# Kernel tuning notes

Measured on AMD Instinct MI355X. Metric: run time of the kernel, lower is better.

## Reference

```python
import jax, jax.numpy as jnp
import numpy as np

N, E = 50000, 600000
NODE_DIM, EDGE_DIM, MSG_DIM = 128, 64, 128


def setup_inputs() -> dict:
    key = jax.random.key(0)
    ks = jax.random.split(key, 8)
    s = 0.05
    return {
        "node_features": jax.random.normal(ks[0], (N, NODE_DIM), jnp.float32),
        "edge_features": jax.random.normal(ks[1], (E, EDGE_DIM), jnp.float32),
        "edge_index": jax.random.randint(ks[2], (2, E), 0, N, jnp.int32),
        "We1": jax.random.normal(ks[3], (2 * NODE_DIM + EDGE_DIM, 32), jnp.float32) * s,
        "be1": jnp.zeros((32,), jnp.float32),
        "We2": jax.random.normal(ks[4], (32, MSG_DIM), jnp.float32) * s,
        "be2": jnp.zeros((MSG_DIM,), jnp.float32),
        "Wn1": jax.random.normal(ks[5], (NODE_DIM + MSG_DIM, 64), jnp.float32) * s,
        "bn1": jnp.zeros((64,), jnp.float32),
        "Wn2": jax.random.normal(ks[6], (64, MSG_DIM), jnp.float32) * s,
        "bn2": jnp.zeros((MSG_DIM,), jnp.float32),
    }


def reference(node_features, edge_features, edge_index,
              We1, be1, We2, be2, Wn1, bn1, Wn2, bn2):
    src, dst = edge_index[0], edge_index[1]
    src_f = node_features[src]            # [E, node_dim] gather
    dst_f = node_features[dst]            # [E, node_dim] gather
    # edge message encoder: 2-layer MLP with ReLU
    edge_in = jnp.concatenate([src_f, dst_f, edge_features], axis=1)  # [E, 2*nd+ed]
    h = jax.nn.relu(edge_in @ We1 + be1)
    edge_msg = jax.nn.relu(h @ We2 + be2)  # [E, msg_dim]
    # node message encoder
    node_in = jnp.concatenate([dst_f, edge_msg], axis=1)  # [E, nd+md]
    h2 = jax.nn.relu(node_in @ Wn1 + bn1)
    node_msg = jax.nn.relu(h2 @ Wn2 + bn2)  # [E, msg_dim]
    # scatter-sum over destination nodes (replaces the O(N) python loop)
    agg = jax.ops.segment_sum(node_msg, dst, num_segments=node_features.shape[0])
    return node_features + agg
```

## Files before the change

### kernel.cpp

```cpp
#include <hip/hip_runtime.h>
#include <hip/hip_bf16.h>

constexpr int N_NODES = 50000;
constexpr int N_EDGES = 600000;
constexpr int ND = 128;
constexpr int ED = 64;
constexpr int MD = 128;
constexpr int H1 = 32;
constexpr int H2 = 64;

typedef __attribute__((ext_vector_type(8))) short short8;
typedef __attribute__((ext_vector_type(4))) float f32x4;

#define MFMA16(a, b, c) __builtin_amdgcn_mfma_f32_16x16x32_bf16((a), (b), (c), 0, 0, 0)

constexpr size_t WS_MSGS    = 0;
constexpr size_t WS_PRE     = WS_MSGS + (size_t)N_EDGES * MD * 2;
constexpr size_t WS_POS     = WS_PRE + (size_t)N_NODES * 128 * 2;
constexpr size_t WS_COUNTS  = WS_POS + (size_t)N_EDGES * 4;
constexpr size_t WS_OFFSETS = WS_COUNTS + (size_t)N_NODES * 4;
constexpr size_t WS_WFE     = ((WS_OFFSETS + (size_t)(N_NODES + 1) * 4 + 15) / 16) * 16;
constexpr size_t WS_WFN     = WS_WFE + (size_t)44 * 64 * 16;
constexpr size_t WS_END     = WS_WFN + (size_t)32 * 64 * 16;

__device__ inline float bflo(unsigned u) { return __uint_as_float(u << 16); }
__device__ inline float bfhi(unsigned u) { return __uint_as_float(u & 0xffff0000u); }
__device__ inline float bf2f(unsigned short v) { return __uint_as_float((unsigned)v << 16); }
__device__ inline short f2bf(float f) {
    __hip_bfloat16 h = __float2bfloat16(f);
    return *reinterpret_cast<short*>(&h);
}

__global__ __launch_bounds__(256) void wprep(
    const float* __restrict__ We1, const float* __restrict__ We2,
    const float* __restrict__ Wn1, const float* __restrict__ Wn2,
    short8* __restrict__ wfE, short8* __restrict__ wfN)
{
    const int g = blockIdx.x * 256 + threadIdx.x;
    const int lane = g & 63;
    const int f = g >> 6;
    const int m16 = lane & 15, quad = lane >> 4;
    short v[8];
    if (f < 44) {
        #pragma unroll
        for (int j = 0; j < 8; ++j) {
            const int kq = quad * 8 + j;
            float s;
            if (f < 4) {
                const int kt = f >> 1, nt = f & 1;
                s = We1[(size_t)(2 * ND + kt * 32 + kq) * H1 + nt * 16 + m16];
            } else if (f < 12) {
                const int nt = f - 4;
                s = We2[(size_t)kq * MD + nt * 16 + m16];
            } else if (f < 28) {
                const int ff = f - 12, kt = ff >> 2, nt = ff & 3;
                s = Wn1[(size_t)(ND + kt * 32 + kq) * H2 + nt * 16 + m16];
            } else {
                const int ff = f - 28, kt = ff >> 3, nt = ff & 7;
                s = Wn2[(size_t)(kt * 32 + kq) * MD + nt * 16 + m16];
            }
            v[j] = f2bf(s);
        }
        wfE[g] = short8{v[0], v[1], v[2], v[3], v[4], v[5], v[6], v[7]};
    } else {
        const int ff = f - 44, kt = ff >> 3, nt = ff & 7;
        const int n = nt * 16 + m16;
        #pragma unroll
        for (int j = 0; j < 8; ++j) {
            const int k = kt * 32 + quad * 8 + j;
            float s;
            if (n < 32)      s = We1[(size_t)k * H1 + n];
            else if (n < 64) s = We1[(size_t)(ND + k) * H1 + (n - 32)];
            else             s = Wn1[(size_t)k * H2 + (n - 64)];
            v[j] = f2bf(s);
        }
        wfN[(size_t)(f - 44) * 64 + lane] = short8{v[0], v[1], v[2], v[3], v[4], v[5], v[6], v[7]};
    }
}

__global__ __launch_bounds__(256) void hist_pos(const int* __restrict__ eidx,
                                                int* __restrict__ counts,
                                                int* __restrict__ pos) {
    const int e = blockIdx.x * 256 + threadIdx.x;
    if (e < N_EDGES) pos[e] = atomicAdd(&counts[eidx[N_EDGES + e]], 1);
}

__global__ __launch_bounds__(1024) void scan_kernel(const int* __restrict__ counts,
                                                    int* __restrict__ offsets) {
    constexpr int T = 1024;
    constexpr int CHUNK = (N_NODES + T - 1) / T;
    const int tid = threadIdx.x;
    const int base = tid * CHUNK;
    int s = 0;
    #pragma unroll
    for (int i = 0; i < CHUNK; ++i) {
        const int idx = base + i;
        if (idx < N_NODES) s += counts[idx];
    }
    __shared__ int sm[T];
    sm[tid] = s;
    __syncthreads();
    for (int off = 1; off < T; off <<= 1) {
        const int v = (tid >= off) ? sm[tid - off] : 0;
        __syncthreads();
        sm[tid] += v;
        __syncthreads();
    }
    int run = sm[tid] - s;
    #pragma unroll
    for (int i = 0; i < CHUNK; ++i) {
        const int idx = base + i;
        if (idx < N_NODES) {
            offsets[idx] = run;
            run += counts[idx];
        }
    }
    if (tid == T - 1) offsets[N_NODES] = sm[T - 1];
}

__global__ __launch_bounds__(256) void node_pre_mfma(
    const float* __restrict__ nf, const short8* __restrict__ wfN,
    unsigned short* __restrict__ pre)
{
    __shared__ short ost[4][2048];
    const int tid = threadIdx.x;
    const int w = tid >> 6, lane = tid & 63;
    const int m16 = lane & 15, quad = lane >> 4;
    const int n0 = blockIdx.x * 64 + w * 16;

    short8 a[4];
    #pragma unroll
    for (int kt = 0; kt < 4; ++kt) {
        const int node = min(n0 + m16, N_NODES - 1);
        const float* pn = nf + (size_t)node * ND + kt * 32 + quad * 8;
        const float4 f0 = *(const float4*)pn;
        const float4 f1 = *(const float4*)(pn + 4);
        a[kt] = short8{f2bf(f0.x), f2bf(f0.y), f2bf(f0.z), f2bf(f0.w),
                       f2bf(f1.x), f2bf(f1.y), f2bf(f1.z), f2bf(f1.w)};
    }
    f32x4 acc[8];
    #pragma unroll
    for (int nt = 0; nt < 8; ++nt) acc[nt] = f32x4{0.f, 0.f, 0.f, 0.f};
    #pragma unroll
    for (int kt = 0; kt < 4; ++kt) {
        #pragma unroll
        for (int nt = 0; nt < 8; ++nt)
            acc[nt] = MFMA16(a[kt], wfN[(size_t)(kt * 8 + nt) * 64 + lane], acc[nt]);
    }
    short* o = &ost[w][0];
    #pragma unroll
    for (int nt = 0; nt < 8; ++nt)
        #pragma unroll
        for (int r = 0; r < 4; ++r)
            o[(quad * 4 + r) * 128 + nt * 16 + m16] = f2bf(acc[nt][r]);
    asm volatile("s_waitcnt lgkmcnt(0)" ::: "memory");
    #pragma unroll
    for (int i = 0; i < 4; ++i) {
        const int row = i * 4 + quad;
        const int node = n0 + row;
        if (node < N_NODES) {
            const uint4 v = ((const uint4*)(o + row * 128))[m16];
            *((uint4*)(pre + (size_t)node * 128) + m16) = v;
        }
    }
}

__global__ __launch_bounds__(256, 4) void edge_mfma(
    const float* __restrict__ ef, const int* __restrict__ eidx,
    const unsigned short* __restrict__ pre,
    const int* __restrict__ pos, const int* __restrict__ offsets,
    const short8* __restrict__ wfE,
    const float* __restrict__ be1, const float* __restrict__ be2,
    const float* __restrict__ bn1, const float* __restrict__ bn2,
    unsigned short* __restrict__ msgs)
{
    constexpr int TE = 64;
    __shared__ float l1init[TE][36];
    __shared__ unsigned short a3lds[TE][72];
    __shared__ int slotlds[TE];
    __shared__ short wbufB[4][2176];

    const int tid = threadIdx.x;
    const int e0 = blockIdx.x * TE;
    const int w = tid >> 6, lane = tid & 63;
    const int m16 = lane & 15, quad = lane >> 4;
    const int er0 = w * 16;

    float4 efv0, efv1, efv2, efv3;
    {
        const float* pe = ef + (size_t)(e0 + er0 + m16) * ED + quad * 8;
        efv0 = *(const float4*)pe;
        efv1 = *(const float4*)(pe + 4);
        efv2 = *(const float4*)(pe + 32);
        efv3 = *(const float4*)(pe + 36);
    }
    float bias2[8], bias3[4], bias4[8];
    #pragma unroll
    for (int nt = 0; nt < 8; ++nt) bias2[nt] = be2[nt * 16 + m16];
    #pragma unroll
    for (int nt = 0; nt < 4; ++nt) bias3[nt] = bn1[nt * 16 + m16];
    #pragma unroll
    for (int nt = 0; nt < 8; ++nt) bias4[nt] = bn2[nt * 16 + m16];

    {
        const int et = tid >> 2, p = tid & 3;
        const int e = e0 + et;
        const int src = eidx[e];
        const int dst = eidx[N_EDGES + e];
        const uint4* pa = (const uint4*)(pre + (size_t)src * 128);
        const uint4* pd = (const uint4*)(pre + (size_t)dst * 128);
        const uint4 ua = pa[p];
        const uint4 ud = pd[4 + p];
        const uint4 s0 = pd[8 + 2 * p];
        const uint4 s1 = pd[9 + 2 * p];
        const float4 b0 = ((const float4*)be1)[2 * p];
        const float4 b1 = ((const float4*)be1)[2 * p + 1];
        float4 r0, r1;
        r0.x = bflo(ua.x) + bflo(ud.x) + b0.x;
        r0.y = bfhi(ua.x) + bfhi(ud.x) + b0.y;
        r0.z = bflo(ua.y) + bflo(ud.y) + b0.z;
        r0.w = bfhi(ua.y) + bfhi(ud.y) + b0.w;
        r1.x = bflo(ua.z) + bflo(ud.z) + b1.x;
        r1.y = bfhi(ua.z) + bfhi(ud.z) + b1.y;
        r1.z = bflo(ua.w) + bflo(ud.w) + b1.z;
        r1.w = bfhi(ua.w) + bfhi(ud.w) + b1.w;
        float4* o = (float4*)&l1init[et][p * 8];
        o[0] = r0; o[1] = r1;
        uint4* oa = (uint4*)&a3lds[et][p * 16];
        oa[0] = s0; oa[1] = s1;
        const int sl = offsets[dst] + pos[e];
        if (p == 3) slotlds[et] = sl;
    }
    asm volatile("s_waitcnt lgkmcnt(0)" ::: "memory");

    short8 aef0 = short8{f2bf(efv0.x), f2bf(efv0.y), f2bf(efv0.z), f2bf(efv0.w),
                         f2bf(efv1.x), f2bf(efv1.y), f2bf(efv1.z), f2bf(efv1.w)};
    short8 aef1 = short8{f2bf(efv2.x), f2bf(efv2.y), f2bf(efv2.z), f2bf(efv2.w),
                         f2bf(efv3.x), f2bf(efv3.y), f2bf(efv3.z), f2bf(efv3.w)};

    short* alb = (short*)&l1init[er0][0];
    short* msb = &wbufB[w][0];

    f32x4 acc1[2];
    #pragma unroll
    for (int nt = 0; nt < 2; ++nt)
        #pragma unroll
        for (int r = 0; r < 4; ++r)
            acc1[nt][r] = l1init[er0 + quad * 4 + r][nt * 16 + m16];
    #pragma unroll
    for (int nt = 0; nt < 2; ++nt) {
        acc1[nt] = MFMA16(aef0, wfE[(size_t)(0 * 2 + nt) * 64 + lane], acc1[nt]);
        acc1[nt] = MFMA16(aef1, wfE[(size_t)(1 * 2 + nt) * 64 + lane], acc1[nt]);
    }
    #pragma unroll
    for (int nt = 0; nt < 2; ++nt)
        #pragma unroll
        for (int r = 0; r < 4; ++r)
            alb[(quad * 4 + r) * 40 + nt * 16 + m16] = f2bf(fmaxf(acc1[nt][r], 0.0f));
    asm volatile("s_waitcnt lgkmcnt(0)" ::: "memory");

    const short8 ah = *(const short8*)(alb + m16 * 40 + quad * 8);
    f32x4 acc2[8];
    #pragma unroll
    for (int nt = 0; nt < 8; ++nt) {
        acc2[nt] = f32x4{bias2[nt], bias2[nt], bias2[nt], bias2[nt]};
        acc2[nt] = MFMA16(ah, wfE[(size_t)(4 + nt) * 64 + lane], acc2[nt]);
    }
    #pragma unroll
    for (int nt = 0; nt < 8; ++nt)
        #pragma unroll
        for (int r = 0; r < 4; ++r)
            msb[(quad * 4 + r) * 136 + nt * 16 + m16] = f2bf(fmaxf(acc2[nt][r], 0.0f));
    asm volatile("s_waitcnt lgkmcnt(0)" ::: "memory");

    short8 am[4];
    #pragma unroll
    for (int kt = 0; kt < 4; ++kt)
        am[kt] = *(const short8*)(msb + m16 * 136 + kt * 32 + quad * 8);
    f32x4 acc3[4];
    #pragma unroll
    for (int nt = 0; nt < 4; ++nt)
        #pragma unroll
        for (int r = 0; r < 4; ++r)
            acc3[nt][r] = bias3[nt] + bf2f(a3lds[er0 + quad * 4 + r][nt * 16 + m16]);
    #pragma unroll
    for (int kt = 0; kt < 4; ++kt) {
        #pragma unroll
        for (int nt = 0; nt < 4; ++nt)
            acc3[nt] = MFMA16(am[kt], wfE[(size_t)(12 + kt * 4 + nt) * 64 + lane], acc3[nt]);
    }
    #pragma unroll
    for (int nt = 0; nt < 4; ++nt)
        #pragma unroll
        for (int r = 0; r < 4; ++r)
            alb[(quad * 4 + r) * 72 + nt * 16 + m16] = f2bf(fmaxf(acc3[nt][r], 0.0f));
    asm volatile("s_waitcnt lgkmcnt(0)" ::: "memory");

    short8 a4[2];
    #pragma unroll
    for (int kt = 0; kt < 2; ++kt)
        a4[kt] = *(const short8*)(alb + m16 * 72 + kt * 32 + quad * 8);
    f32x4 acc4[8];
    #pragma unroll
    for (int nt = 0; nt < 8; ++nt)
        acc4[nt] = f32x4{bias4[nt], bias4[nt], bias4[nt], bias4[nt]};
    #pragma unroll
    for (int kt = 0; kt < 2; ++kt) {
        #pragma unroll
        for (int nt = 0; nt < 8; ++nt)
            acc4[nt] = MFMA16(a4[kt], wfE[(size_t)(28 + kt * 8 + nt) * 64 + lane], acc4[nt]);
    }
    #pragma unroll
    for (int nt = 0; nt < 8; ++nt)
        #pragma unroll
        for (int r = 0; r < 4; ++r)
            msb[(quad * 4 + r) * 128 + nt * 16 + m16] = f2bf(fmaxf(acc4[nt][r], 0.0f));
    asm volatile("s_waitcnt lgkmcnt(0)" ::: "memory");

    #pragma unroll
    for (int i = 0; i < 4; ++i) {
        const int row = i * 4 + quad;
        const int sl = slotlds[er0 + row];
        const uint4 v = ((const uint4*)(msb + row * 128))[m16];
        *((uint4*)(msgs + (size_t)sl * 128) + m16) = v;
    }
}

__global__ __launch_bounds__(256) void gather2(
    const float* __restrict__ nf,
    const uint4* __restrict__ msgs4,
    const int* __restrict__ offsets,
    float* __restrict__ out)
{
    const int node = blockIdx.x * 16 + (threadIdx.x >> 4);
    const int m16 = threadIdx.x & 15;

    const float4* pn = (const float4*)(nf + (size_t)node * ND) + m16 * 2;
    const float4 n0 = pn[0];
    const float4 n1 = pn[1];

    const int beg = offsets[node];
    const int end = offsets[node + 1];

    float4 s0 = float4{0.f, 0.f, 0.f, 0.f};
    float4 s1 = float4{0.f, 0.f, 0.f, 0.f};
    const uint4* p = msgs4 + (size_t)beg * 16 + m16;
    int i = beg;
    for (; i + 1 < end; i += 2, p += 32) {
        const uint4 u0 = p[0];
        const uint4 u1 = p[16];
        s0.x += bflo(u0.x); s0.y += bfhi(u0.x);
        s0.z += bflo(u0.y); s0.w += bfhi(u0.y);
        s1.x += bflo(u0.z); s1.y += bfhi(u0.z);
        s1.z += bflo(u0.w); s1.w += bfhi(u0.w);
        s0.x += bflo(u1.x); s0.y += bfhi(u1.x);
        s0.z += bflo(u1.y); s0.w += bfhi(u1.y);
        s1.x += bflo(u1.z); s1.y += bfhi(u1.z);
        s1.z += bflo(u1.w); s1.w += bfhi(u1.w);
    }
    if (i < end) {
        const uint4 u = p[0];
        s0.x += bflo(u.x); s0.y += bfhi(u.x);
        s0.z += bflo(u.y); s0.w += bfhi(u.y);
        s1.x += bflo(u.z); s1.y += bfhi(u.z);
        s1.z += bflo(u.w); s1.w += bfhi(u.w);
    }
    s0.x += n0.x; s0.y += n0.y; s0.z += n0.z; s0.w += n0.w;
    s1.x += n1.x; s1.y += n1.y; s1.z += n1.z; s1.w += n1.w;

    float4* po = (float4*)(out + (size_t)node * ND) + m16 * 2;
    po[0] = s0;
    po[1] = s1;
}

extern "C" void kernel_launch(void* const* d_in, const int* in_sizes, int n_in,
                              void* d_out, int out_size, void* d_ws, size_t ws_size,
                              hipStream_t stream) {
    const float* nf  = (const float*)d_in[0];
    const float* ef  = (const float*)d_in[1];
    const int*  eidx = (const int*)d_in[2];
    const float* We1 = (const float*)d_in[3];
    const float* be1 = (const float*)d_in[4];
    const float* We2 = (const float*)d_in[5];
    const float* be2 = (const float*)d_in[6];
    const float* Wn1 = (const float*)d_in[7];
    const float* bn1 = (const float*)d_in[8];
    const float* Wn2 = (const float*)d_in[9];
    const float* bn2 = (const float*)d_in[10];
    float* out = (float*)d_out;

    char* ws = (char*)d_ws;
    unsigned short* msgs = (unsigned short*)(ws + WS_MSGS);
    unsigned short* pre  = (unsigned short*)(ws + WS_PRE);
    int* pos             = (int*)(ws + WS_POS);
    int* counts          = (int*)(ws + WS_COUNTS);
    int* offsets         = (int*)(ws + WS_OFFSETS);
    short8* wfE          = (short8*)(ws + WS_WFE);
    short8* wfN          = (short8*)(ws + WS_WFN);
    (void)ws_size; (void)WS_END;

    hipMemsetAsync(counts, 0, (size_t)N_NODES * 4, stream);
    wprep<<<19, 256, 0, stream>>>(We1, We2, Wn1, Wn2, wfE, wfN);
    hist_pos<<<(N_EDGES + 255) / 256, 256, 0, stream>>>(eidx, counts, pos);
    scan_kernel<<<1, 1024, 0, stream>>>(counts, offsets);
    node_pre_mfma<<<(N_NODES + 63) / 64, 256, 0, stream>>>(nf, wfN, pre);
    edge_mfma<<<N_EDGES / 64, 256, 0, stream>>>(
        ef, eidx, pre, pos, offsets, wfE, be1, be2, bn1, bn2, msgs);
    gather2<<<N_NODES / 16, 256, 0, stream>>>(nf, (const uint4*)msgs, offsets, out);
}
```

Measured before the change: 494.4 us.

## Transpose edge MLP MFMAs to keep activations in registers between layers

The edge MLP now swaps the MFMA operand roles: weights become the A operand and activations the B operand. Combined with a permuted K ordering of the weights in wprep, each layer's ReLU'd output feeds the next layer directly from registers instead of round-tripping through LDS. This cuts LDS traffic, waitcnts and shared memory, and occupancy is raised to 5 waves per SIMD. Packed bf16 conversion instructions replace scalar conversions. The scan is vectorised with padded counts, at the cost of tighter register pressure and a more intricate index mapping.

```diff
diff --git a/kernel.cpp b/kernel.cpp
--- a/kernel.cpp
+++ b/kernel.cpp
@@ -11,24 +11,41 @@
 
 typedef __attribute__((ext_vector_type(8))) short short8;
 typedef __attribute__((ext_vector_type(4))) float f32x4;
+typedef __attribute__((ext_vector_type(4))) unsigned int uint32x4;
 
 #define MFMA16(a, b, c) __builtin_amdgcn_mfma_f32_16x16x32_bf16((a), (b), (c), 0, 0, 0)
 
+constexpr int COUNTS_PAD = 53248;
 constexpr size_t WS_MSGS    = 0;
 constexpr size_t WS_PRE     = WS_MSGS + (size_t)N_EDGES * MD * 2;
 constexpr size_t WS_POS     = WS_PRE + (size_t)N_NODES * 128 * 2;
 constexpr size_t WS_COUNTS  = WS_POS + (size_t)N_EDGES * 4;
-constexpr size_t WS_OFFSETS = WS_COUNTS + (size_t)N_NODES * 4;
+constexpr size_t WS_OFFSETS = WS_COUNTS + (size_t)COUNTS_PAD * 4;
 constexpr size_t WS_WFE     = ((WS_OFFSETS + (size_t)(N_NODES + 1) * 4 + 15) / 16) * 16;
 constexpr size_t WS_WFN     = WS_WFE + (size_t)44 * 64 * 16;
 constexpr size_t WS_END     = WS_WFN + (size_t)32 * 64 * 16;
 
 __device__ inline float bflo(unsigned u) { return __uint_as_float(u << 16); }
 __device__ inline float bfhi(unsigned u) { return __uint_as_float(u & 0xffff0000u); }
-__device__ inline float bf2f(unsigned short v) { return __uint_as_float((unsigned)v << 16); }
 __device__ inline short f2bf(float f) {
     __hip_bfloat16 h = __float2bfloat16(f);
     return *reinterpret_cast<short*>(&h);
+}
+__device__ inline unsigned pkbf(float a, float b) {
+    unsigned r;
+    asm("v_cvt_pk_bf16_f32 %0, %1, %2" : "=v"(r) : "v"(a), "v"(b));
+    return r;
+}
+__device__ inline unsigned prelu(float a, float b) {
+    return pkbf(fmaxf(a, 0.0f), fmaxf(b, 0.0f));
+}
+__device__ inline short8 pack8(unsigned w0, unsigned w1, unsigned w2, unsigned w3) {
+    uint32x4 t{w0, w1, w2, w3};
+    return __builtin_bit_cast(short8, t);
+}
+
+__device__ inline int hperm(int kt, int kq) {
+    return (kt * 2 + ((kq >> 2) & 1)) * 16 + ((kq >> 3) & 3) * 4 + (kq & 3);
 }
 
 __global__ __launch_bounds__(256) void wprep(
@@ -47,17 +64,17 @@
             const int kq = quad * 8 + j;
             float s;
             if (f < 4) {
-                const int kt = f >> 1, nt = f & 1;
-                s = We1[(size_t)(2 * ND + kt * 32 + kq) * H1 + nt * 16 + m16];
+                const int kt = f >> 1, mt = f & 1;
+                s = We1[(size_t)(2 * ND + kt * 32 + kq) * H1 + mt * 16 + m16];
             } else if (f < 12) {
-                const int nt = f - 4;
-                s = We2[(size_t)kq * MD + nt * 16 + m16];
+                const int mt = f - 4;
+                s = We2[(size_t)hperm(0, kq) * MD + mt * 16 + m16];
             } else if (f < 28) {
-                const int ff = f - 12, kt = ff >> 2, nt = ff & 3;
-                s = Wn1[(size_t)(ND + kt * 32 + kq) * H2 + nt * 16 + m16];
+                const int ff = f - 12, kt = ff >> 2, mt = ff & 3;
+                s = Wn1[(size_t)(ND + hperm(kt, kq)) * H2 + mt * 16 + m16];
             } else {
-                const int ff = f - 28, kt = ff >> 3, nt = ff & 7;
-                s = Wn2[(size_t)(kt * 32 + kq) * MD + nt * 16 + m16];
+                const int ff = f - 28, kt = ff >> 3, mt = ff & 7;
+                s = Wn2[(size_t)hperm(kt, kq) * MD + mt * 16 + m16];
             }
             v[j] = f2bf(s);
         }
@@ -88,34 +105,35 @@
 __global__ __launch_bounds__(1024) void scan_kernel(const int* __restrict__ counts,
                                                     int* __restrict__ offsets) {
     constexpr int T = 1024;
-    constexpr int CHUNK = (N_NODES + T - 1) / T;
+    constexpr int CHUNK = 52;
     const int tid = threadIdx.x;
     const int base = tid * CHUNK;
+    int4 v[13];
     int s = 0;
-    #pragma unroll
-    for (int i = 0; i < CHUNK; ++i) {
-        const int idx = base + i;
-        if (idx < N_NODES) s += counts[idx];
+    const int4* pc = (const int4*)(counts + base);
+    #pragma unroll
+    for (int i = 0; i < 13; ++i) {
+        v[i] = pc[i];
+        s += v[i].x + v[i].y + v[i].z + v[i].w;
     }
     __shared__ int sm[T];
     sm[tid] = s;
     __syncthreads();
     for (int off = 1; off < T; off <<= 1) {
-        const int v = (tid >= off) ? sm[tid - off] : 0;
+        const int t = (tid >= off) ? sm[tid - off] : 0;
         __syncthreads();
-        sm[tid] += v;
+        sm[tid] += t;
         __syncthreads();
     }
     int run = sm[tid] - s;
     #pragma unroll
-    for (int i = 0; i < CHUNK; ++i) {
-        const int idx = base + i;
-        if (idx < N_NODES) {
-            offsets[idx] = run;
-            run += counts[idx];
-        }
-    }
-    if (tid == T - 1) offsets[N_NODES] = sm[T - 1];
+    for (int i = 0; i < 13; ++i) {
+        const int idx = base + i * 4;
+        if (idx     <= N_NODES) offsets[idx]     = run;  run += v[i].x;
+        if (idx + 1 <= N_NODES) offsets[idx + 1] = run;  run += v[i].y;
+        if (idx + 2 <= N_NODES) offsets[idx + 2] = run;  run += v[i].z;
+        if (idx + 3 <= N_NODES) offsets[idx + 3] = run;  run += v[i].w;
+    }
 }
 
 __global__ __launch_bounds__(256) void node_pre_mfma(
@@ -135,8 +153,8 @@
         const float* pn = nf + (size_t)node * ND + kt * 32 + quad * 8;
         const float4 f0 = *(const float4*)pn;
         const float4 f1 = *(const float4*)(pn + 4);
-        a[kt] = short8{f2bf(f0.x), f2bf(f0.y), f2bf(f0.z), f2bf(f0.w),
-                       f2bf(f1.x), f2bf(f1.y), f2bf(f1.z), f2bf(f1.w)};
+        a[kt] = pack8(pkbf(f0.x, f0.y), pkbf(f0.z, f0.w),
+                      pkbf(f1.x, f1.y), pkbf(f1.z, f1.w));
     }
     f32x4 acc[8];
     #pragma unroll
@@ -165,7 +183,7 @@
     }
 }
 
-__global__ __launch_bounds__(256, 4) void edge_mfma(
+__global__ __launch_bounds__(256, 5) void edge_mfma(
     const float* __restrict__ ef, const int* __restrict__ eidx,
     const unsigned short* __restrict__ pre,
     const int* __restrict__ pos, const int* __restrict__ offsets,
@@ -175,32 +193,24 @@
     unsigned short* __restrict__ msgs)
 {
     constexpr int TE = 64;
-    __shared__ float l1init[TE][36];
-    __shared__ unsigned short a3lds[TE][72];
+    __shared__ __align__(16) char sws[4][4608];
     __shared__ int slotlds[TE];
-    __shared__ short wbufB[4][2176];
 
     const int tid = threadIdx.x;
     const int e0 = blockIdx.x * TE;
     const int w = tid >> 6, lane = tid & 63;
-    const int m16 = lane & 15, quad = lane >> 4;
+    const int m16 = lane & 15, q = lane >> 4;
     const int er0 = w * 16;
+    char* swsb = &sws[w][0];
 
     float4 efv0, efv1, efv2, efv3;
     {
-        const float* pe = ef + (size_t)(e0 + er0 + m16) * ED + quad * 8;
+        const float* pe = ef + (size_t)(e0 + er0 + m16) * ED + q * 8;
         efv0 = *(const float4*)pe;
         efv1 = *(const float4*)(pe + 4);
         efv2 = *(const float4*)(pe + 32);
         efv3 = *(const float4*)(pe + 36);
     }
-    float bias2[8], bias3[4], bias4[8];
-    #pragma unroll
-    for (int nt = 0; nt < 8; ++nt) bias2[nt] = be2[nt * 16 + m16];
-    #pragma unroll
-    for (int nt = 0; nt < 4; ++nt) bias3[nt] = bn1[nt * 16 + m16];
-    #pragma unroll
-    for (int nt = 0; nt < 8; ++nt) bias4[nt] = bn2[nt * 16 + m16];
 
     {
         const int et = tid >> 2, p = tid & 3;
@@ -224,104 +234,98 @@
         r1.y = bfhi(ua.z) + bfhi(ud.z) + b1.y;
         r1.z = bflo(ua.w) + bflo(ud.w) + b1.z;
         r1.w = bfhi(ua.w) + bfhi(ud.w) + b1.w;
-        float4* o = (float4*)&l1init[et][p * 8];
-        o[0] = r0; o[1] = r1;
-        uint4* oa = (uint4*)&a3lds[et][p * 16];
-        oa[0] = s0; oa[1] = s1;
-        const int sl = offsets[dst] + pos[e];
-        if (p == 3) slotlds[et] = sl;
+        char* wb = &sws[et >> 4][0] + (et & 15) * 144;
+        *(float4*)(wb + p * 32) = r0;
+        *(float4*)(wb + p * 32 + 16) = r1;
+        char* wb2 = &sws[et >> 4][2304] + (et & 15) * 144;
+        *(uint4*)(wb2 + p * 32) = s0;
+        *(uint4*)(wb2 + p * 32 + 16) = s1;
+        if (p == 3) slotlds[et] = offsets[dst] + pos[e];
     }
     asm volatile("s_waitcnt lgkmcnt(0)" ::: "memory");
 
-    short8 aef0 = short8{f2bf(efv0.x), f2bf(efv0.y), f2bf(efv0.z), f2bf(efv0.w),
-                         f2bf(efv1.x), f2bf(efv1.y), f2bf(efv1.z), f2bf(efv1.w)};
-    short8 aef1 = short8{f2bf(efv2.x), f2bf(efv2.y), f2bf(efv2.z), f2bf(efv2.w),
-                         f2bf(efv3.x), f2bf(efv3.y), f2bf(efv3.z), f2bf(efv3.w)};
-
-    short* alb = (short*)&l1init[er0][0];
-    short* msb = &wbufB[w][0];
+    const short8 aef0 = pack8(pkbf(efv0.x, efv0.y), pkbf(efv0.z, efv0.w),
+                              pkbf(efv1.x, efv1.y), pkbf(efv1.z, efv1.w));
+    const short8 aef1 = pack8(pkbf(efv2.x, efv2.y), pkbf(efv2.z, efv2.w),
+                              pkbf(efv3.x, efv3.y), pkbf(efv3.z, efv3.w));
 
     f32x4 acc1[2];
     #pragma unroll
-    for (int nt = 0; nt < 2; ++nt)
-        #pragma unroll
-        for (int r = 0; r < 4; ++r)
-            acc1[nt][r] = l1init[er0 + quad * 4 + r][nt * 16 + m16];
-    #pragma unroll
-    for (int nt = 0; nt < 2; ++nt) {
-        acc1[nt] = MFMA16(aef0, wfE[(size_t)(0 * 2 + nt) * 64 + lane], acc1[nt]);
-        acc1[nt] = MFMA16(aef1, wfE[(size_t)(1 * 2 + nt) * 64 + lane], acc1[nt]);
-    }
-    #pragma unroll
-    for (int nt = 0; nt < 2; ++nt)
-        #pragma unroll
-        for (int r = 0; r < 4; ++r)
-            alb[(quad * 4 + r) * 40 + nt * 16 + m16] = f2bf(fmaxf(acc1[nt][r], 0.0f));
+    for (int mt = 0; mt < 2; ++mt)
+        acc1[mt] = *(const f32x4*)(swsb + m16 * 144 + mt * 64 + q * 16);
+    #pragma unroll
+    for (int mt = 0; mt < 2; ++mt) {
+        acc1[mt] = MFMA16(wfE[(size_t)(0 + mt) * 64 + lane], aef0, acc1[mt]);
+        acc1[mt] = MFMA16(wfE[(size_t)(2 + mt) * 64 + lane], aef1, acc1[mt]);
+    }
+
+    const short8 b2 = pack8(prelu(acc1[0][0], acc1[0][1]), prelu(acc1[0][2], acc1[0][3]),
+                            prelu(acc1[1][0], acc1[1][1]), prelu(acc1[1][2], acc1[1][3]));
+
+    f32x4 acc2[8];
+    #pragma unroll
+    for (int mt = 0; mt < 8; ++mt) {
+        const float4 bb = *(const float4*)(be2 + mt * 16 + q * 4);
+        acc2[mt] = f32x4{bb.x, bb.y, bb.z, bb.w};
+        acc2[mt] = MFMA16(wfE[(size_t)(4 + mt) * 64 + lane], b2, acc2[mt]);
+    }
+    short8 b3[4];
+    #pragma unroll
+    for (int kt = 0; kt < 4; ++kt)
+        b3[kt] = pack8(prelu(acc2[2 * kt][0], acc2[2 * kt][1]),
+                       prelu(acc2[2 * kt][2], acc2[2 * kt][3]),
+                       prelu(acc2[2 * kt + 1][0], acc2[2 * kt + 1][1]),
+                       prelu(acc2[2 * kt + 1][2], acc2[2 * kt + 1][3]));
+
+    f32x4 acc3[4];
+    #pragma unroll
+    for (int mt = 0; mt < 4; ++mt) {
+        const float4 bb = *(const float4*)(bn1 + mt * 16 + q * 4);
+        const uint2 ua = *(const uint2*)(swsb + 2304 + m16 * 144 + mt * 32 + q * 8);
+        acc3[mt] = f32x4{bb.x + bflo(ua.x), bb.y + bfhi(ua.x),
+                         bb.z + bflo(ua.y), bb.w + bfhi(ua.y)};
+    }
+    #pragma unroll
+    for (int kt = 0; kt < 4; ++kt) {
+        #pragma unroll
+        for (int mt = 0; mt < 4; ++mt)
+            acc3[mt] = MFMA16(wfE[(size_t)(12 + kt * 4 + mt) * 64 + lane], b3[kt], acc3[mt]);
+    }
+    short8 b4[2];
+    #pragma unroll
+    for (int kt = 0; kt < 2; ++kt)
+        b4[kt] = pack8(prelu(acc3[2 * kt][0], acc3[2 * kt][1]),
+                       prelu(acc3[2 * kt][2], acc3[2 * kt][3]),
+                       prelu(acc3[2 * kt + 1][0], acc3[2 * kt + 1][1]),
+                       prelu(acc3[2 * kt + 1][2], acc3[2 * kt + 1][3]));
+
+    f32x4 acc4[8];
+    #pragma unroll
+    for (int mt = 0; mt < 8; ++mt) {
+        const float4 bb = *(const float4*)(bn2 + mt * 16 + q * 4);
+        acc4[mt] = f32x4{bb.x, bb.y, bb.z, bb.w};
+    }
+    #pragma unroll
+    for (int kt = 0; kt < 2; ++kt) {
+        #pragma unroll
+        for (int mt = 0; mt < 8; ++mt)
+            acc4[mt] = MFMA16(wfE[(size_t)(28 + kt * 8 + mt) * 64 + lane], b4[kt], acc4[mt]);
+    }
+
+    #pragma unroll
+    for (int mt = 0; mt < 8; ++mt) {
+        uint2 wv;
+        wv.x = prelu(acc4[mt][0], acc4[mt][1]);
+        wv.y = prelu(acc4[mt][2], acc4[mt][3]);
+        *(uint2*)(swsb + m16 * 272 + mt * 32 + q * 8) = wv;
+    }
     asm volatile("s_waitcnt lgkmcnt(0)" ::: "memory");
 
-    const short8 ah = *(const short8*)(alb + m16 * 40 + quad * 8);
-    f32x4 acc2[8];
-    #pragma unroll
-    for (int nt = 0; nt < 8; ++nt) {
-        acc2[nt] = f32x4{bias2[nt], bias2[nt], bias2[nt], bias2[nt]};
-        acc2[nt] = MFMA16(ah, wfE[(size_t)(4 + nt) * 64 + lane], acc2[nt]);
-    }
-    #pragma unroll
-    for (int nt = 0; nt < 8; ++nt)
-        #pragma unroll
-        for (int r = 0; r < 4; ++r)
-            msb[(quad * 4 + r) * 136 + nt * 16 + m16] = f2bf(fmaxf(acc2[nt][r], 0.0f));
-    asm volatile("s_waitcnt lgkmcnt(0)" ::: "memory");
-
-    short8 am[4];
-    #pragma unroll
-    for (int kt = 0; kt < 4; ++kt)
-        am[kt] = *(const short8*)(msb + m16 * 136 + kt * 32 + quad * 8);
-    f32x4 acc3[4];
-    #pragma unroll
-    for (int nt = 0; nt < 4; ++nt)
-        #pragma unroll
-        for (int r = 0; r < 4; ++r)
-            acc3[nt][r] = bias3[nt] + bf2f(a3lds[er0 + quad * 4 + r][nt * 16 + m16]);
-    #pragma unroll
-    for (int kt = 0; kt < 4; ++kt) {
-        #pragma unroll
-        for (int nt = 0; nt < 4; ++nt)
-            acc3[nt] = MFMA16(am[kt], wfE[(size_t)(12 + kt * 4 + nt) * 64 + lane], acc3[nt]);
-    }
-    #pragma unroll
-    for (int nt = 0; nt < 4; ++nt)
-        #pragma unroll
-        for (int r = 0; r < 4; ++r)
-            alb[(quad * 4 + r) * 72 + nt * 16 + m16] = f2bf(fmaxf(acc3[nt][r], 0.0f));
-    asm volatile("s_waitcnt lgkmcnt(0)" ::: "memory");
-
-    short8 a4[2];
-    #pragma unroll
-    for (int kt = 0; kt < 2; ++kt)
-        a4[kt] = *(const short8*)(alb + m16 * 72 + kt * 32 + quad * 8);
-    f32x4 acc4[8];
-    #pragma unroll
-    for (int nt = 0; nt < 8; ++nt)
-        acc4[nt] = f32x4{bias4[nt], bias4[nt], bias4[nt], bias4[nt]};
-    #pragma unroll
-    for (int kt = 0; kt < 2; ++kt) {
-        #pragma unroll
-        for (int nt = 0; nt < 8; ++nt)
-            acc4[nt] = MFMA16(a4[kt], wfE[(size_t)(28 + kt * 8 + nt) * 64 + lane], acc4[nt]);
-    }
-    #pragma unroll
-    for (int nt = 0; nt < 8; ++nt)
-        #pragma unroll
-        for (int r = 0; r < 4; ++r)
-            msb[(quad * 4 + r) * 128 + nt * 16 + m16] = f2bf(fmaxf(acc4[nt][r], 0.0f));
-    asm volatile("s_waitcnt lgkmcnt(0)" ::: "memory");
-
     #pragma unroll
     for (int i = 0; i < 4; ++i) {
-        const int row = i * 4 + quad;
+        const int row = i * 4 + q;
         const int sl = slotlds[er0 + row];
-        const uint4 v = ((const uint4*)(msb + row * 128))[m16];
+        const uint4 v = *(const uint4*)(swsb + row * 272 + m16 * 16);
         *((uint4*)(msgs + (size_t)sl * 128) + m16) = v;
     }
 }
@@ -399,7 +403,7 @@
     short8* wfN          = (short8*)(ws + WS_WFN);
     (void)ws_size; (void)WS_END;
 
-    hipMemsetAsync(counts, 0, (size_t)N_NODES * 4, stream);
+    hipMemsetAsync(counts, 0, (size_t)COUNTS_PAD * 4, stream);
     wprep<<<19, 256, 0, stream>>>(We1, We2, Wn1, Wn2, wfE, wfN);
     hist_pos<<<(N_EDGES + 255) / 256, 256, 0, stream>>>(eidx, counts, pos);
     scan_kernel<<<1, 1024, 0, stream>>>(counts, offsets);
```

New measurement: 459.2 us. -7.1%, faster.
